# Kernel tuning notes

Hardware: AMD Instinct MI355X
Metric: run time of the kernel (lower is better)

Reference implementation:

```python
import jax, jax.numpy as jnp
import numpy as np

HIDDEN = 256
IN = 72  # 9*8
NUM_STEPS = 8


def setup_inputs() -> dict:
    key = jax.random.key(0)
    ks = jax.random.split(key, 12)
    s = 1.0 / np.sqrt(HIDDEN)
    B = 32768
    return {
        "z": jax.random.normal(ks[0], (1, B, HIDDEN), dtype=jnp.float32),
        # LSTM (torch layout): gates order i, f, g, o
        "W_ih": jax.random.uniform(ks[1], (4 * HIDDEN, IN), minval=-s, maxval=s),
        "W_hh": jax.random.uniform(ks[2], (4 * HIDDEN, HIDDEN), minval=-s, maxval=s),
        "b_ih": jax.random.uniform(ks[3], (4 * HIDDEN,), minval=-s, maxval=s),
        "b_hh": jax.random.uniform(ks[4], (4 * HIDDEN,), minval=-s, maxval=s),
        # Linear h: 256 -> 256
        "Wh": jax.random.uniform(ks[5], (HIDDEN, HIDDEN), minval=-s, maxval=s),
        "bh": jax.random.uniform(ks[6], (HIDDEN,), minval=-s, maxval=s),
        # Linear c: 256 -> 256
        "Wc": jax.random.uniform(ks[7], (HIDDEN, HIDDEN), minval=-s, maxval=s),
        "bc": jax.random.uniform(ks[8], (HIDDEN,), minval=-s, maxval=s),
        # Linear hout: 256 -> 72
        "Wo": jax.random.uniform(ks[9], (IN, HIDDEN), minval=-s, maxval=s),
        "bo": jax.random.uniform(ks[10], (IN,), minval=-s, maxval=s),
    }


def reference(z, W_ih, W_hh, b_ih, b_hh, Wh, bh, Wc, bc, Wo, bo):
    B = z.shape[1]
    z0 = z[0]                           # (B, 256)
    h = z0 @ Wh.T + bh                  # initial hidden state
    c = z0 @ Wc.T + bc                  # initial cell state
    x = jnp.zeros((B, IN), dtype=z.dtype)

    def step(carry, _):
        x, h, c = carry
        gates = x @ W_ih.T + b_ih + h @ W_hh.T + b_hh   # (B, 1024)
        i, f, g, o = jnp.split(gates, 4, axis=-1)
        i = jax.nn.sigmoid(i)
        f = jax.nn.sigmoid(f)
        g = jnp.tanh(g)
        o = jax.nn.sigmoid(o)
        c = f * c + i * g
        h = o * jnp.tanh(c)
        y = jax.nn.sigmoid(h @ Wo.T + bo)               # (B, 72), fed back as next input
        return (y, h, c), y

    _, ys = jax.lax.scan(step, (x, h, c), None, length=NUM_STEPS)  # (8, B, 72)
    return jnp.transpose(ys, (1, 0, 2))                             # (B, 8, 72)
```

## Files before the change

kernel.cpp:

```cpp
#include <hip/hip_runtime.h>
#include <hip/hip_bf16.h>

#define HID   256
#define NGATE 1024
#define INP   72
#define INPP  96
#define STEPS 8
#define TB    64
#define LDH   264
#define LDX   104

#define OFF_WHH 0
#define OFF_WIH 262144
#define OFF_WH  360448
#define OFF_WC  425984
#define OFF_WO  491520
#define N_BF    512000
#define OFF_BG_BYTES 1024000
#define OFF_STAGE_BYTES (1u << 20)

typedef short  s8_t  __attribute__((ext_vector_type(8)));
typedef float  f4_t  __attribute__((ext_vector_type(4)));

static __device__ __forceinline__ unsigned short f2bf(float f) {
  unsigned int u = __float_as_uint(f);
  u = (u + 0x7FFFu + ((u >> 16) & 1u)) >> 16;
  return (unsigned short)u;
}
static __device__ __forceinline__ float fast_rcp(float x) {
#if __has_builtin(__builtin_amdgcn_rcpf)
  return __builtin_amdgcn_rcpf(x);
#else
  return 1.f / x;
#endif
}
static __device__ __forceinline__ float sigm(float x) {
  return fast_rcp(1.f + __expf(-x));
}
static __device__ __forceinline__ float tanh_(float x) {
  float t = fminf(-2.f * x, 88.f);
  float e = __expf(t);
  return (1.f - e) * fast_rcp(1.f + e);
}

__global__ void prep_kernel(const float* __restrict__ Wih, const float* __restrict__ Whh,
                            const float* __restrict__ bih, const float* __restrict__ bhh,
                            const float* __restrict__ Wh, const float* __restrict__ Wc,
                            const float* __restrict__ Wo,
                            unsigned short* __restrict__ wsh, float* __restrict__ bg) {
  int stride = gridDim.x * blockDim.x;
  for (int i = blockIdx.x * blockDim.x + threadIdx.x; i < N_BF + NGATE; i += stride) {
    if (i < N_BF) {
      int e    = i & 511;
      int fiA  = i >> 9;
      int lane = e >> 3;
      int j    = e & 7;
      int lq   = lane >> 4;
      int ln   = lane & 15;
      int kk   = lq * 8 + j;
      float v  = 0.f;
      if (i < OFF_WIH) {
        int fi = fiA;
        int kc = fi & 7, t = fi >> 3, ct = t & 1, u = t >> 1, q = u & 3, w = u >> 2;
        int g  = q * 256 + w * 32 + ct * 16 + ln;
        int k  = kc * 32 + kk;
        v = Whh[g * HID + k];
      } else if (i < OFF_WH) {
        int fi = fiA - (OFF_WIH >> 9);
        int kc = fi % 3, t = fi / 3, ct = t & 1, u = t >> 1, q = u & 3, w = u >> 2;
        int g  = q * 256 + w * 32 + ct * 16 + ln;
        int k  = kc * 32 + kk;
        v = (k < INP) ? Wih[g * INP + k] : 0.f;
      } else if (i < OFF_WC) {
        int fi = fiA - (OFF_WH >> 9);
        int kc = fi & 7, t = fi >> 3, ct = t & 1, w = t >> 1;
        int c  = w * 32 + ct * 16 + ln;
        int k  = kc * 32 + kk;
        v = Wh[c * HID + k];
      } else if (i < OFF_WO) {
        int fi = fiA - (OFF_WC >> 9);
        int kc = fi & 7, t = fi >> 3, ct = t & 1, w = t >> 1;
        int c  = w * 32 + ct * 16 + ln;
        int k  = kc * 32 + kk;
        v = Wc[c * HID + k];
      } else {
        int fi = fiA - (OFF_WO >> 9);
        int kc = fi & 7, yt = fi >> 3;
        int c  = yt * 16 + ln;
        int k  = kc * 32 + kk;
        v = (c < INP) ? Wo[c * HID + k] : 0.f;
      }
      wsh[i] = f2bf(v);
    } else {
      int jb = i - N_BF;
      bg[jb] = bih[jb] + bhh[jb];
    }
  }
}

template <int STAGED>
__global__ __launch_bounds__(512, 2) void lstm_kernel(
    const float* __restrict__ z, const unsigned short* __restrict__ wsh,
    const float* __restrict__ bg, const float* __restrict__ bh,
    const float* __restrict__ bc, const float* __restrict__ bo,
    float* __restrict__ out, float* __restrict__ stage, int NB) {
  __shared__ unsigned short h_lds[TB * LDH];
  __shared__ unsigned short x_lds[TB * LDX];

  const int tid  = threadIdx.x;
  const int w    = tid >> 6;
  const int lane = tid & 63;
  const int lq   = lane >> 4;
  const int ln   = lane & 15;
  const int rb   = blockIdx.x * TB;
  const int colh0 = w * 32 + ln;

  const unsigned short* whh_l = wsh + OFF_WHH + w * 32768 + lane * 8;
  const unsigned short* wih_l = wsh + OFF_WIH + w * 12288 + lane * 8;
  const unsigned short* wh_l  = wsh + OFF_WH  + w * 8192  + lane * 8;
  const unsigned short* wc_l  = wsh + OFF_WC  + w * 8192  + lane * 8;
  const unsigned short* h_rd  = &h_lds[ln * LDH + lq * 8];
  const unsigned short* x_rd  = &x_lds[ln * LDX + lq * 8];
  unsigned short*       h_wr  = &h_lds[(lq * 4) * LDH + colh0];

  for (int i = tid; i < TB * LDX; i += 512) x_lds[i] = 0;

  f4_t acc_h[4][2], acc_c[4][2];
  #pragma unroll
  for (int rt = 0; rt < 4; ++rt)
    #pragma unroll
    for (int ct = 0; ct < 2; ++ct) {
      acc_h[rt][ct] = {0.f, 0.f, 0.f, 0.f};
      acc_c[rt][ct] = {0.f, 0.f, 0.f, 0.f};
    }

  const float* z_l = z + (size_t)(rb + ln) * HID + lq * 8;

  #pragma unroll 2
  for (int kc = 0; kc < 8; ++kc) {
    s8_t a[4];
    #pragma unroll
    for (int rt = 0; rt < 4; ++rt) {
      f4_t v0 = *reinterpret_cast<const f4_t*>(z_l + rt * 16 * HID + kc * 32);
      f4_t v1 = *reinterpret_cast<const f4_t*>(z_l + rt * 16 * HID + kc * 32 + 4);
      s8_t av;
      av[0] = (short)f2bf(v0[0]); av[1] = (short)f2bf(v0[1]);
      av[2] = (short)f2bf(v0[2]); av[3] = (short)f2bf(v0[3]);
      av[4] = (short)f2bf(v1[0]); av[5] = (short)f2bf(v1[1]);
      av[6] = (short)f2bf(v1[2]); av[7] = (short)f2bf(v1[3]);
      a[rt] = av;
    }
    #pragma unroll
    for (int ct = 0; ct < 2; ++ct) {
      s8_t bhf = *reinterpret_cast<const s8_t*>(wh_l + (ct * 8 + kc) * 512);
      s8_t bcf = *reinterpret_cast<const s8_t*>(wc_l + (ct * 8 + kc) * 512);
      #pragma unroll
      for (int rt = 0; rt < 4; ++rt) {
        acc_h[rt][ct] = __builtin_amdgcn_mfma_f32_16x16x32_bf16(a[rt], bhf, acc_h[rt][ct], 0, 0, 0);
        acc_c[rt][ct] = __builtin_amdgcn_mfma_f32_16x16x32_bf16(a[rt], bcf, acc_c[rt][ct], 0, 0, 0);
      }
    }
  }

  float c_reg[4][2][4];
  #pragma unroll
  for (int ct = 0; ct < 2; ++ct) {
    const float bhv = bh[colh0 + ct * 16];
    const float bcv = bc[colh0 + ct * 16];
    #pragma unroll
    for (int rt = 0; rt < 4; ++rt)
      #pragma unroll
      for (int r = 0; r < 4; ++r) {
        float hv = acc_h[rt][ct][r] + bhv;
        c_reg[rt][ct][r] = acc_c[rt][ct][r] + bcv;
        h_wr[(rt * 16 + r) * LDH + ct * 16] = f2bf(hv);
      }
  }
  __syncthreads();

  float biasg[4][2];
  #pragma unroll
  for (int q = 0; q < 4; ++q)
    #pragma unroll
    for (int ct = 0; ct < 2; ++ct)
      biasg[q][ct] = bg[q * 256 + colh0 + ct * 16];

  const int colY = w * 16 + ln;
  float bov = 0.f;
  const unsigned short* wo_l = wsh + OFF_WO + (w < 5 ? w : 0) * 4096 + lane * 8;
  if (w < 5) {
    if (colY < INP) bov = bo[colY];
  }

  for (int s = 0; s < STEPS; ++s) {
    f4_t acc[4][4][2];
    #pragma unroll
    for (int q = 0; q < 4; ++q)
      #pragma unroll
      for (int rt = 0; rt < 4; ++rt)
        #pragma unroll
        for (int ct = 0; ct < 2; ++ct) {
          const float b = biasg[q][ct];
          acc[q][rt][ct] = {b, b, b, b};
        }

    #pragma unroll 2
    for (int kc = 0; kc < 8; ++kc) {
      s8_t a[4];
      #pragma unroll
      for (int rt = 0; rt < 4; ++rt)
        a[rt] = *reinterpret_cast<const s8_t*>(h_rd + rt * 16 * LDH + kc * 32);
      #pragma unroll
      for (int q = 0; q < 4; ++q)
        #pragma unroll
        for (int ct = 0; ct < 2; ++ct) {
          s8_t bfr = *reinterpret_cast<const s8_t*>(whh_l + (q * 16 + ct * 8 + kc) * 512);
          #pragma unroll
          for (int rt = 0; rt < 4; ++rt)
            acc[q][rt][ct] = __builtin_amdgcn_mfma_f32_16x16x32_bf16(a[rt], bfr, acc[q][rt][ct], 0, 0, 0);
        }
    }
    #pragma unroll
    for (int kc = 0; kc < 3; ++kc) {
      s8_t a[4];
      #pragma unroll
      for (int rt = 0; rt < 4; ++rt)
        a[rt] = *reinterpret_cast<const s8_t*>(x_rd + rt * 16 * LDX + kc * 32);
      #pragma unroll
      for (int q = 0; q < 4; ++q)
        #pragma unroll
        for (int ct = 0; ct < 2; ++ct) {
          s8_t bfr = *reinterpret_cast<const s8_t*>(wih_l + (q * 6 + ct * 3 + kc) * 512);
          #pragma unroll
          for (int rt = 0; rt < 4; ++rt)
            acc[q][rt][ct] = __builtin_amdgcn_mfma_f32_16x16x32_bf16(a[rt], bfr, acc[q][rt][ct], 0, 0, 0);
        }
    }
    __syncthreads();

    #pragma unroll
    for (int rt = 0; rt < 4; ++rt)
      #pragma unroll
      for (int ct = 0; ct < 2; ++ct)
        #pragma unroll
        for (int r = 0; r < 4; ++r) {
          float iv = sigm(acc[0][rt][ct][r]);
          float fv = sigm(acc[1][rt][ct][r]);
          float gv = tanh_(acc[2][rt][ct][r]);
          float ov = sigm(acc[3][rt][ct][r]);
          float cn = fv * c_reg[rt][ct][r] + iv * gv;
          c_reg[rt][ct][r] = cn;
          float hv = ov * tanh_(cn);
          h_wr[(rt * 16 + r) * LDH + ct * 16] = f2bf(hv);
        }
    __syncthreads();

    if (w < 5) {
      f4_t accy[4];
      #pragma unroll
      for (int rt = 0; rt < 4; ++rt) accy[rt] = {bov, bov, bov, bov};
      #pragma unroll 2
      for (int kc = 0; kc < 8; ++kc) {
        s8_t bfr = *reinterpret_cast<const s8_t*>(wo_l + kc * 512);
        #pragma unroll
        for (int rt = 0; rt < 4; ++rt) {
          s8_t a = *reinterpret_cast<const s8_t*>(h_rd + rt * 16 * LDH + kc * 32);
          accy[rt] = __builtin_amdgcn_mfma_f32_16x16x32_bf16(a, bfr, accy[rt], 0, 0, 0);
        }
      }
      if (colY < INP) {
        float* st_base;
        if (STAGED) {
          st_base = stage + (((size_t)s * NB + blockIdx.x) * TB + lq * 4) * INP + colY;
        } else {
          st_base = out + (size_t)(rb + lq * 4) * (STEPS * INP) + s * INP + colY;
        }
        unsigned short* x_wr = &x_lds[(lq * 4) * LDX + colY];
        #pragma unroll
        for (int rt = 0; rt < 4; ++rt)
          #pragma unroll
          for (int r = 0; r < 4; ++r) {
            float yv = sigm(accy[rt][r]);
            if (STAGED) {
              st_base[(size_t)(rt * 16 + r) * INP] = yv;
            } else {
              st_base[(size_t)(rt * 16 + r) * (STEPS * INP)] = yv;
            }
            x_wr[(rt * 16 + r) * LDX] = f2bf(yv);
          }
      }
    }
    __syncthreads();
  }
}

__global__ __launch_bounds__(512) void reorder_kernel(
    const float* __restrict__ stage, float* __restrict__ out, int NB) {
  const int lane = threadIdx.x & 63;
  const int row  = blockIdx.x * 8 + (threadIdx.x >> 6);
  const int b    = row >> 6;
  const int r    = row & 63;
  #pragma unroll
  for (int i = lane; i < STEPS * INP; i += 64) {
    int s = i / INP;
    int c = i - s * INP;
    out[(size_t)row * (STEPS * INP) + i] =
        stage[(((size_t)s * NB + b) * TB + r) * INP + c];
  }
}

extern "C" void kernel_launch(void* const* d_in, const int* in_sizes, int n_in,
                              void* d_out, int out_size, void* d_ws, size_t ws_size,
                              hipStream_t stream) {
  const float* z   = (const float*)d_in[0];
  const float* Wih = (const float*)d_in[1];
  const float* Whh = (const float*)d_in[2];
  const float* bih = (const float*)d_in[3];
  const float* bhh = (const float*)d_in[4];
  const float* Wh  = (const float*)d_in[5];
  const float* bh  = (const float*)d_in[6];
  const float* Wc  = (const float*)d_in[7];
  const float* bc  = (const float*)d_in[8];
  const float* Wo  = (const float*)d_in[9];
  const float* bo  = (const float*)d_in[10];
  float* out = (float*)d_out;

  unsigned short* wsh = (unsigned short*)d_ws;
  float* bg    = (float*)((char*)d_ws + OFF_BG_BYTES);
  float* stage = (float*)((char*)d_ws + OFF_STAGE_BYTES);

  const int B  = in_sizes[0] / HID;
  const int NB = B / TB;

  hipLaunchKernelGGL(prep_kernel, dim3(512), dim3(256), 0, stream,
                     Wih, Whh, bih, bhh, Wh, Wc, Wo, wsh, bg);

  const size_t stage_need = (size_t)OFF_STAGE_BYTES + (size_t)B * STEPS * INP * 4;
  if (ws_size >= stage_need) {
    hipLaunchKernelGGL((lstm_kernel<1>), dim3(NB), dim3(512), 0, stream,
                       z, wsh, bg, bh, bc, bo, out, stage, NB);
    hipLaunchKernelGGL(reorder_kernel, dim3(B / 8), dim3(512), 0, stream,
                       stage, out, NB);
  } else {
    hipLaunchKernelGGL((lstm_kernel<0>), dim3(NB), dim3(512), 0, stream,
                       z, wsh, bg, bh, bc, bo, out, stage, NB);
  }
}
```

Measured before the change: 656.2 us.

## Stream recurrent weights through per-wave LDS ring via async global_load_lds

Repacks all per-wave weights (W_hh, W_ih, Wo) into one contiguous per-wave sequence. Each step streams them through a 12-slot LDS ring using global_load_lds, with vmcnt-based waits, so global loads are issued about 11 fragments ahead of the MFMAs that use them. The aim is to hide global and L2 latency of weight fetches in the recurrent loop, which were previously loaded straight into registers. It also swaps __syncthreads for a custom barrier and fully unrolls the loops. This adds LDS pressure (about 96KB extra), which may lower occupancy below the two-blocks-per-CU launch bound. It also has waves 5-7 issue useless loads in the output phase.

```diff
diff --git a/kernel.cpp b/kernel.cpp
--- a/kernel.cpp
+++ b/kernel.cpp
@@ -4,20 +4,19 @@
 #define HID   256
 #define NGATE 1024
 #define INP   72
-#define INPP  96
 #define STEPS 8
 #define TB    64
 #define LDH   264
 #define LDX   104
 
-#define OFF_WHH 0
-#define OFF_WIH 262144
-#define OFF_WH  360448
-#define OFF_WC  425984
-#define OFF_WO  491520
-#define N_BF    512000
-#define OFF_BG_BYTES 1024000
-#define OFF_STAGE_BYTES (1u << 20)
+#define NFRAG 96
+#define RING  12
+#define WSEQ  49152
+#define OFF_WH2 393216
+#define OFF_WC2 458752
+#define N_ALL   524288
+#define OFF_BG_BYTES    1048576
+#define OFF_STAGE_BYTES 1114112
 
 typedef short  s8_t  __attribute__((ext_vector_type(8)));
 typedef float  f4_t  __attribute__((ext_vector_type(4)));
@@ -43,56 +42,66 @@
   return (1.f - e) * fast_rcp(1.f + e);
 }
 
+#define ISSUE(F, S) __builtin_amdgcn_global_load_lds( \
+    (const __attribute__((address_space(1))) unsigned int*)(const void*)(seq_l + (F) * 512), \
+    (__attribute__((address_space(3))) unsigned int*)(void*)(ring_wr + (S) * 512), 16, 0, 0)
+#define WAITV10() asm volatile("s_waitcnt vmcnt(10)" ::: "memory")
+#define BAR() do { asm volatile("s_waitcnt lgkmcnt(0)" ::: "memory"); \
+                   __builtin_amdgcn_s_barrier(); \
+                   asm volatile("" ::: "memory"); } while (0)
+
 __global__ void prep_kernel(const float* __restrict__ Wih, const float* __restrict__ Whh,
                             const float* __restrict__ bih, const float* __restrict__ bhh,
                             const float* __restrict__ Wh, const float* __restrict__ Wc,
                             const float* __restrict__ Wo,
                             unsigned short* __restrict__ wsh, float* __restrict__ bg) {
   int stride = gridDim.x * blockDim.x;
-  for (int i = blockIdx.x * blockDim.x + threadIdx.x; i < N_BF + NGATE; i += stride) {
-    if (i < N_BF) {
-      int e    = i & 511;
-      int fiA  = i >> 9;
-      int lane = e >> 3;
-      int j    = e & 7;
-      int lq   = lane >> 4;
-      int ln   = lane & 15;
-      int kk   = lq * 8 + j;
-      float v  = 0.f;
-      if (i < OFF_WIH) {
-        int fi = fiA;
-        int kc = fi & 7, t = fi >> 3, ct = t & 1, u = t >> 1, q = u & 3, w = u >> 2;
-        int g  = q * 256 + w * 32 + ct * 16 + ln;
-        int k  = kc * 32 + kk;
-        v = Whh[g * HID + k];
-      } else if (i < OFF_WH) {
-        int fi = fiA - (OFF_WIH >> 9);
-        int kc = fi % 3, t = fi / 3, ct = t & 1, u = t >> 1, q = u & 3, w = u >> 2;
-        int g  = q * 256 + w * 32 + ct * 16 + ln;
-        int k  = kc * 32 + kk;
-        v = (k < INP) ? Wih[g * INP + k] : 0.f;
-      } else if (i < OFF_WC) {
-        int fi = fiA - (OFF_WH >> 9);
-        int kc = fi & 7, t = fi >> 3, ct = t & 1, w = t >> 1;
+  for (int i = blockIdx.x * blockDim.x + threadIdx.x; i < N_ALL + NGATE; i += stride) {
+    if (i < N_ALL) {
+      float v = 0.f;
+      if (i < OFF_WH2) {
+        int w  = i / WSEQ;
+        int r  = i - w * WSEQ;
+        int f  = r >> 9;
+        int e  = r & 511;
+        int lane = e >> 3, j = e & 7;
+        int lq = lane >> 4, ln = lane & 15;
+        int kk = lq * 8 + j;
+        if (f < 64) {
+          int kc = f >> 3, t = f & 7, q = t >> 1, ct = t & 1;
+          int g  = q * 256 + w * 32 + ct * 16 + ln;
+          int k  = kc * 32 + kk;
+          v = Whh[g * HID + k];
+        } else if (f < 88) {
+          int t2 = f - 64;
+          int kc = t2 >> 3, t = t2 & 7, q = t >> 1, ct = t & 1;
+          int g  = q * 256 + w * 32 + ct * 16 + ln;
+          int k  = kc * 32 + kk;
+          v = (k < INP) ? Wih[g * INP + k] : 0.f;
+        } else {
+          int kc = f - 88;
+          int c  = w * 16 + ln;
+          int k  = kc * 32 + kk;
+          v = (w < 5 && c < INP) ? Wo[c * HID + k] : 0.f;
+        }
+      } else {
+        int base = (i < OFF_WC2) ? OFF_WH2 : OFF_WC2;
+        const float* Wsrc = (i < OFF_WC2) ? Wh : Wc;
+        int jj = i - base;
+        int w  = jj >> 13;
+        int r  = jj & 8191;
+        int fi = r >> 9;
+        int e  = r & 511;
+        int lane = e >> 3, j = e & 7;
+        int lq = lane >> 4, ln = lane & 15;
+        int ct = fi >> 3, kc = fi & 7;
         int c  = w * 32 + ct * 16 + ln;
-        int k  = kc * 32 + kk;
-        v = Wh[c * HID + k];
-      } else if (i < OFF_WO) {
-        int fi = fiA - (OFF_WC >> 9);
-        int kc = fi & 7, t = fi >> 3, ct = t & 1, w = t >> 1;
-        int c  = w * 32 + ct * 16 + ln;
-        int k  = kc * 32 + kk;
-        v = Wc[c * HID + k];
-      } else {
-        int fi = fiA - (OFF_WO >> 9);
-        int kc = fi & 7, yt = fi >> 3;
-        int c  = yt * 16 + ln;
-        int k  = kc * 32 + kk;
-        v = (c < INP) ? Wo[c * HID + k] : 0.f;
+        int k  = kc * 32 + lq * 8 + j;
+        v = Wsrc[c * HID + k];
       }
       wsh[i] = f2bf(v);
     } else {
-      int jb = i - N_BF;
+      int jb = i - N_ALL;
       bg[jb] = bih[jb] + bhh[jb];
     }
   }
@@ -106,6 +115,7 @@
     float* __restrict__ out, float* __restrict__ stage, int NB) {
   __shared__ unsigned short h_lds[TB * LDH];
   __shared__ unsigned short x_lds[TB * LDX];
+  __shared__ unsigned short ring[8 * RING * 512];
 
   const int tid  = threadIdx.x;
   const int w    = tid >> 6;
@@ -115,13 +125,15 @@
   const int rb   = blockIdx.x * TB;
   const int colh0 = w * 32 + ln;
 
-  const unsigned short* whh_l = wsh + OFF_WHH + w * 32768 + lane * 8;
-  const unsigned short* wih_l = wsh + OFF_WIH + w * 12288 + lane * 8;
-  const unsigned short* wh_l  = wsh + OFF_WH  + w * 8192  + lane * 8;
-  const unsigned short* wc_l  = wsh + OFF_WC  + w * 8192  + lane * 8;
-  const unsigned short* h_rd  = &h_lds[ln * LDH + lq * 8];
-  const unsigned short* x_rd  = &x_lds[ln * LDX + lq * 8];
-  unsigned short*       h_wr  = &h_lds[(lq * 4) * LDH + colh0];
+  const unsigned short* seq_l  = wsh + w * WSEQ + lane * 8;
+  unsigned short*       ring_wr = &ring[w * (RING * 512)];
+  const unsigned short* ring_rd = &ring[w * (RING * 512) + lane * 8];
+
+  const unsigned short* wh_l = wsh + OFF_WH2 + w * 8192 + lane * 8;
+  const unsigned short* wc_l = wsh + OFF_WC2 + w * 8192 + lane * 8;
+  const unsigned short* h_rd = &h_lds[ln * LDH + lq * 8];
+  const unsigned short* x_rd = &x_lds[ln * LDX + lq * 8];
+  unsigned short*       h_wr = &h_lds[(lq * 4) * LDH + colh0];
 
   for (int i = tid; i < TB * LDX; i += 512) x_lds[i] = 0;
 
@@ -162,6 +174,9 @@
     }
   }
 
+  #pragma unroll
+  for (int p = 0; p <= 10; ++p) ISSUE(p, p);
+
   float c_reg[4][2][4];
   #pragma unroll
   for (int ct = 0; ct < 2; ++ct) {
@@ -176,7 +191,6 @@
         h_wr[(rt * 16 + r) * LDH + ct * 16] = f2bf(hv);
       }
   }
-  __syncthreads();
 
   float biasg[4][2];
   #pragma unroll
@@ -187,10 +201,13 @@
 
   const int colY = w * 16 + ln;
   float bov = 0.f;
-  const unsigned short* wo_l = wsh + OFF_WO + (w < 5 ? w : 0) * 4096 + lane * 8;
-  if (w < 5) {
-    if (colY < INP) bov = bo[colY];
-  }
+  if (w < 5 && colY < INP) bov = bo[colY];
+
+  BAR();
+
+  WAITV10();
+  s8_t bcur = *reinterpret_cast<const s8_t*>(ring_rd);
+  s8_t bnxt;
 
   for (int s = 0; s < STEPS; ++s) {
     f4_t acc[4][4][2];
@@ -204,7 +221,7 @@
           acc[q][rt][ct] = {b, b, b, b};
         }
 
-    #pragma unroll 2
+    #pragma unroll
     for (int kc = 0; kc < 8; ++kc) {
       s8_t a[4];
       #pragma unroll
@@ -214,10 +231,14 @@
       for (int q = 0; q < 4; ++q)
         #pragma unroll
         for (int ct = 0; ct < 2; ++ct) {
-          s8_t bfr = *reinterpret_cast<const s8_t*>(whh_l + (q * 16 + ct * 8 + kc) * 512);
+          const int f = kc * 8 + q * 2 + ct;
+          ISSUE((f + 11) % NFRAG, (f + 11) % RING);
+          WAITV10();
+          bnxt = *reinterpret_cast<const s8_t*>(ring_rd + ((f + 1) % RING) * 512);
           #pragma unroll
           for (int rt = 0; rt < 4; ++rt)
-            acc[q][rt][ct] = __builtin_amdgcn_mfma_f32_16x16x32_bf16(a[rt], bfr, acc[q][rt][ct], 0, 0, 0);
+            acc[q][rt][ct] = __builtin_amdgcn_mfma_f32_16x16x32_bf16(a[rt], bcur, acc[q][rt][ct], 0, 0, 0);
+          bcur = bnxt;
         }
     }
     #pragma unroll
@@ -230,13 +251,17 @@
       for (int q = 0; q < 4; ++q)
         #pragma unroll
         for (int ct = 0; ct < 2; ++ct) {
-          s8_t bfr = *reinterpret_cast<const s8_t*>(wih_l + (q * 6 + ct * 3 + kc) * 512);
+          const int f = 64 + kc * 8 + q * 2 + ct;
+          ISSUE((f + 11) % NFRAG, (f + 11) % RING);
+          WAITV10();
+          bnxt = *reinterpret_cast<const s8_t*>(ring_rd + ((f + 1) % RING) * 512);
           #pragma unroll
           for (int rt = 0; rt < 4; ++rt)
-            acc[q][rt][ct] = __builtin_amdgcn_mfma_f32_16x16x32_bf16(a[rt], bfr, acc[q][rt][ct], 0, 0, 0);
-        }
-    }
-    __syncthreads();
+            acc[q][rt][ct] = __builtin_amdgcn_mfma_f32_16x16x32_bf16(a[rt], bcur, acc[q][rt][ct], 0, 0, 0);
+          bcur = bnxt;
+        }
+    }
+    BAR();
 
     #pragma unroll
     for (int rt = 0; rt < 4; ++rt)
@@ -253,22 +278,28 @@
           float hv = ov * tanh_(cn);
           h_wr[(rt * 16 + r) * LDH + ct * 16] = f2bf(hv);
         }
-    __syncthreads();
-
-    if (w < 5) {
+    BAR();
+
+    {
       f4_t accy[4];
       #pragma unroll
       for (int rt = 0; rt < 4; ++rt) accy[rt] = {bov, bov, bov, bov};
-      #pragma unroll 2
+      #pragma unroll
       for (int kc = 0; kc < 8; ++kc) {
-        s8_t bfr = *reinterpret_cast<const s8_t*>(wo_l + kc * 512);
-        #pragma unroll
-        for (int rt = 0; rt < 4; ++rt) {
-          s8_t a = *reinterpret_cast<const s8_t*>(h_rd + rt * 16 * LDH + kc * 32);
-          accy[rt] = __builtin_amdgcn_mfma_f32_16x16x32_bf16(a, bfr, accy[rt], 0, 0, 0);
-        }
-      }
-      if (colY < INP) {
+        const int f = 88 + kc;
+        ISSUE((f + 11) % NFRAG, (f + 11) % RING);
+        WAITV10();
+        bnxt = *reinterpret_cast<const s8_t*>(ring_rd + ((f + 1) % RING) * 512);
+        if (w < 5) {
+          #pragma unroll
+          for (int rt = 0; rt < 4; ++rt) {
+            s8_t a = *reinterpret_cast<const s8_t*>(h_rd + rt * 16 * LDH + kc * 32);
+            accy[rt] = __builtin_amdgcn_mfma_f32_16x16x32_bf16(a, bcur, accy[rt], 0, 0, 0);
+          }
+        }
+        bcur = bnxt;
+      }
+      if (w < 5 && colY < INP) {
         float* st_base;
         if (STAGED) {
           st_base = stage + (((size_t)s * NB + blockIdx.x) * TB + lq * 4) * INP + colY;
@@ -290,7 +321,7 @@
           }
       }
     }
-    __syncthreads();
+    BAR();
   }
 }
 
```

Measured after the change: 869.6 us. +32.5%, slower.
